# Performance work log

Hardware: AMD Instinct MI355X
Metric: run time of the kernel (lower is better)

Reference implementation:

```python
import jax, jax.numpy as jnp
import numpy as np

GROUP = 32  # quantization group size along K, fixed by the call site


def setup_inputs() -> dict:
    key = jax.random.key(0)
    k1, k2, k3 = jax.random.split(key, 3)
    M, K, N = 1, 8192, 16384
    A = jax.random.normal(k1, (M, K), dtype=jnp.float16)
    # packed int4 weights: each byte holds two nibbles -> [N, K//2]
    B = jax.random.randint(k2, (N, K // 2), 0, 256, dtype=jnp.int32)
    scalesAndZeros = (jax.random.normal(k3, (N, K // GROUP, 2), dtype=jnp.float16))
    return {"A": A, "B": B, "scalesAndZeros": scalesAndZeros}


def _dequant(B, scalesAndZeros):
    # B: [N, K//2] bytes, two int4 values per byte (low nibble = even k)
    N, Kh = B.shape
    K = Kh * 2
    low = B & 0xF
    high = (B >> 4) & 0xF
    q = jnp.stack([low, high], axis=-1).reshape(N, K).astype(jnp.float32) - 8.0
    scales = scalesAndZeros[..., 0].astype(jnp.float32)  # [N, K//GROUP]
    zeros = scalesAndZeros[..., 1].astype(jnp.float32)   # [N, K//GROUP]
    qg = q.reshape(N, K // GROUP, GROUP)
    W = qg * scales[:, :, None] + zeros[:, :, None]       # [N, K//GROUP, GROUP]
    return W.reshape(N, K)


def reference(A, B, scalesAndZeros):
    # int4 weight-only quantized GEMV: out[m, n] = sum_k A[m, k] * dequant(W)[n, k]
    W = _dequant(B, scalesAndZeros)                        # [N, K] fp32
    out = jnp.einsum("mk,nk->mn", A.astype(jnp.float32), W)
    return out.astype(A.dtype)                             # [1, N] fp16
```

## Files before the change

kernel.cpp:

```cpp
#include <hip/hip_runtime.h>


#define TPB   512
#define ROWS  2
#define TILES 16
#define CROWS (ROWS * TILES)

typedef int   ivec4 __attribute__((ext_vector_type(4)));
typedef float fvec2 __attribute__((ext_vector_type(2)));

__global__ __launch_bounds__(TPB, 4) void gemv_w4pipe(
    const float4* __restrict__ A4,
    const ivec4*  __restrict__ B,
    const fvec2*  __restrict__ SZ,
    float* __restrict__ out,
    int N)
{
    const int t    = threadIdx.x;
    const int row0 = blockIdx.x * CROWS;
    const int g0   = t >> 2;

    __shared__ fvec2 sz_s[2][ROWS * 256];
    __shared__ float red[2][ROWS][TPB / 64];

    float a[2][8];
    float sA[2];
#pragma unroll
    for (int j = 0; j < 2; ++j) {
        const int i = t + 512 * j;
        const float4 x = A4[2 * i];
        const float4 y = A4[2 * i + 1];
        a[j][0] = x.x; a[j][1] = x.y; a[j][2] = x.z; a[j][3] = x.w;
        a[j][4] = y.x; a[j][5] = y.y; a[j][6] = y.z; a[j][7] = y.w;
        sA[j] = ((x.x + x.y) + (x.z + x.w)) + ((y.x + y.y) + (y.z + y.w));
    }

    ivec4 bufA[ROWS][2], bufB[ROWS][2];
    fvec2 szrA, szrB;

    auto issue = [&](int T, ivec4 (&buf)[ROWS][2], fvec2& szr) {
        const int rt = row0 + T * ROWS;
        szr = __builtin_nontemporal_load(&SZ[(size_t)rt * 256 + t]);
        const ivec4* Bp = B + (size_t)rt * 1024 + t;
#pragma unroll
        for (int r = 0; r < ROWS; ++r)
#pragma unroll
            for (int j = 0; j < 2; ++j)
                buf[r][j] = __builtin_nontemporal_load(&Bp[r * 1024 + 512 * j]);
    };

    auto consume = [&](const ivec4 (&buf)[ROWS][2], const fvec2* szl,
                       float (&redb)[ROWS][TPB / 64]) {
        float acc[ROWS];
#pragma unroll
        for (int r = 0; r < ROWS; ++r) acc[r] = 0.0f;
#pragma unroll
        for (int r = 0; r < ROWS; ++r) {
#pragma unroll
            for (int j = 0; j < 2; ++j) {
                const fvec2 sz = szl[r * 256 + g0 + 128 * j];
                const int b0 = buf[r][j][0], b1 = buf[r][j][1];
                const int b2 = buf[r][j][2], b3 = buf[r][j][3];
                float dot = 0.0f;
                dot = fmaf(a[j][0], (float)(b0 & 0xF),        dot);
                dot = fmaf(a[j][1], (float)((b0 >> 4) & 0xF), dot);
                dot = fmaf(a[j][2], (float)(b1 & 0xF),        dot);
                dot = fmaf(a[j][3], (float)((b1 >> 4) & 0xF), dot);
                dot = fmaf(a[j][4], (float)(b2 & 0xF),        dot);
                dot = fmaf(a[j][5], (float)((b2 >> 4) & 0xF), dot);
                dot = fmaf(a[j][6], (float)(b3 & 0xF),        dot);
                dot = fmaf(a[j][7], (float)((b3 >> 4) & 0xF), dot);
                acc[r] = fmaf(sz[0], dot, acc[r]);
                acc[r] = fmaf(fmaf(-8.0f, sz[0], sz[1]), sA[j], acc[r]);
            }
        }
        const int lane = t & 63;
        const int w    = t >> 6;
#pragma unroll
        for (int r = 0; r < ROWS; ++r) {
            float v = acc[r];
#pragma unroll
            for (int off = 32; off > 0; off >>= 1)
                v += __shfl_down(v, off, 64);
            if (lane == 0) redb[r][w] = v;
        }
    };

    auto store2 = [&](int T, const float (&redb)[ROWS][TPB / 64]) {
        if (t < ROWS) {
            const int n = row0 + T * ROWS + t;
            if (n < N) {
                float v = 0.0f;
#pragma unroll
                for (int w2 = 0; w2 < TPB / 64; ++w2) v += redb[t][w2];
                out[n] = v;
            }
        }
    };

    issue(0, bufA, szrA);
    sz_s[0][t] = szrA;
    __syncthreads();

    for (int TT = 0; TT < TILES; TT += 2) {
        if (TT + 1 < TILES) issue(TT + 1, bufB, szrB);
        consume(bufA, &sz_s[0][0], red[0]);
        if (TT + 1 < TILES) sz_s[1][t] = szrB;
        __syncthreads();
        store2(TT, red[0]);

        if (TT + 2 < TILES) issue(TT + 2, bufA, szrA);
        consume(bufB, &sz_s[1][0], red[1]);
        if (TT + 2 < TILES) sz_s[0][t] = szrA;
        __syncthreads();
        store2(TT + 1, red[1]);
    }
}

extern "C" void kernel_launch(void* const* d_in, const int* in_sizes, int n_in,
                              void* d_out, int out_size, void* d_ws, size_t ws_size,
                              hipStream_t stream) {
    const float4* A4 = (const float4*)d_in[0];
    const ivec4*  B  = (const ivec4*)d_in[1];
    const fvec2*  SZ = (const fvec2*)d_in[2];
    float* out = (float*)d_out;

    const int N = out_size;
    gemv_w4pipe<<<N / CROWS, TPB, 0, stream>>>(A4, B, SZ, out, N);
}
```

Baseline: 351.5 us.

## Replace LDS-staged scales and per-tile barriers with register double-buffered asm loads

Scales and zeros are now loaded straight into registers by each thread instead of being staged through shared memory. The per-tile __syncthreads barriers are removed, leaving a single barrier before a final 32-row reduction. Weight and scale loads go through inline asm (nontemporal dwordx4 and dwordx2) with explicit vmcnt waits, so two tiles stay in flight per thread. This aims to cut barrier stalls and LDS traffic, at the cost of redundant scale loads across threads and a fragile hand-counted vmcnt scheme.

```diff
diff --git a/kernel.cpp b/kernel.cpp
--- a/kernel.cpp
+++ b/kernel.cpp
@@ -9,7 +9,14 @@
 typedef int   ivec4 __attribute__((ext_vector_type(4)));
 typedef float fvec2 __attribute__((ext_vector_type(2)));
 
-__global__ __launch_bounds__(TPB, 4) void gemv_w4pipe(
+#define NT16(dst, p) asm volatile("global_load_dwordx4 %0, %1, off sc0 sc1 nt" \
+                                  : "=v"(dst) : "v"(p) : "memory")
+#define LD8(dst, p)  asm volatile("global_load_dwordx2 %0, %1, off"            \
+                                  : "=v"(dst) : "v"(p) : "memory")
+#define WAITV(n)     do { asm volatile("s_waitcnt vmcnt(" n ")" ::: "memory"); \
+                          __builtin_amdgcn_sched_barrier(0); } while (0)
+
+__global__ __launch_bounds__(TPB, 4) void gemv_w4str(
     const float4* __restrict__ A4,
     const ivec4*  __restrict__ B,
     const fvec2*  __restrict__ SZ,
@@ -17,14 +24,15 @@
     int N)
 {
     const int t    = threadIdx.x;
+    const int lane = t & 63;
+    const int w    = t >> 6;
     const int row0 = blockIdx.x * CROWS;
     const int g0   = t >> 2;
 
-    __shared__ fvec2 sz_s[2][ROWS * 256];
-    __shared__ float red[2][ROWS][TPB / 64];
+    __shared__ float red2[CROWS][8];
 
     float a[2][8];
-    float sA[2];
+    float sAv[2];
 #pragma unroll
     for (int j = 0; j < 2; ++j) {
         const int i = t + 512 * j;
@@ -32,25 +40,27 @@
         const float4 y = A4[2 * i + 1];
         a[j][0] = x.x; a[j][1] = x.y; a[j][2] = x.z; a[j][3] = x.w;
         a[j][4] = y.x; a[j][5] = y.y; a[j][6] = y.z; a[j][7] = y.w;
-        sA[j] = ((x.x + x.y) + (x.z + x.w)) + ((y.x + y.y) + (y.z + y.w));
+        sAv[j] = ((x.x + x.y) + (x.z + x.w)) + ((y.x + y.y) + (y.z + y.w));
     }
 
-    ivec4 bufA[ROWS][2], bufB[ROWS][2];
-    fvec2 szrA, szrB;
+    ivec4 bA[4], bB[4];
+    fvec2 szA[4], szB[4];
 
-    auto issue = [&](int T, ivec4 (&buf)[ROWS][2], fvec2& szr) {
+    auto issue = [&](int T, ivec4 (&b)[4], fvec2 (&sz)[4]) {
         const int rt = row0 + T * ROWS;
-        szr = __builtin_nontemporal_load(&SZ[(size_t)rt * 256 + t]);
         const ivec4* Bp = B + (size_t)rt * 1024 + t;
-#pragma unroll
-        for (int r = 0; r < ROWS; ++r)
-#pragma unroll
-            for (int j = 0; j < 2; ++j)
-                buf[r][j] = __builtin_nontemporal_load(&Bp[r * 1024 + 512 * j]);
+        NT16(b[0], Bp);
+        NT16(b[1], Bp + 512);
+        NT16(b[2], Bp + 1024);
+        NT16(b[3], Bp + 1536);
+        const fvec2* Sp = SZ + (size_t)rt * 256 + g0;
+        LD8(sz[0], Sp);
+        LD8(sz[1], Sp + 128);
+        LD8(sz[2], Sp + 256);
+        LD8(sz[3], Sp + 384);
     };
 
-    auto consume = [&](const ivec4 (&buf)[ROWS][2], const fvec2* szl,
-                       float (&redb)[ROWS][TPB / 64]) {
+    auto consume = [&](const ivec4 (&b)[4], const fvec2 (&sz)[4], int rr) {
         float acc[ROWS];
 #pragma unroll
         for (int r = 0; r < ROWS; ++r) acc[r] = 0.0f;
@@ -58,62 +68,54 @@
         for (int r = 0; r < ROWS; ++r) {
 #pragma unroll
             for (int j = 0; j < 2; ++j) {
-                const fvec2 sz = szl[r * 256 + g0 + 128 * j];
-                const int b0 = buf[r][j][0], b1 = buf[r][j][1];
-                const int b2 = buf[r][j][2], b3 = buf[r][j][3];
+                const ivec4 bb = b[r * 2 + j];
+                const fvec2 ss = sz[r * 2 + j];
+                const int c0 = bb[0], c1 = bb[1], c2 = bb[2], c3 = bb[3];
                 float dot = 0.0f;
-                dot = fmaf(a[j][0], (float)(b0 & 0xF),        dot);
-                dot = fmaf(a[j][1], (float)((b0 >> 4) & 0xF), dot);
-                dot = fmaf(a[j][2], (float)(b1 & 0xF),        dot);
-                dot = fmaf(a[j][3], (float)((b1 >> 4) & 0xF), dot);
-                dot = fmaf(a[j][4], (float)(b2 & 0xF),        dot);
-                dot = fmaf(a[j][5], (float)((b2 >> 4) & 0xF), dot);
-                dot = fmaf(a[j][6], (float)(b3 & 0xF),        dot);
-                dot = fmaf(a[j][7], (float)((b3 >> 4) & 0xF), dot);
-                acc[r] = fmaf(sz[0], dot, acc[r]);
-                acc[r] = fmaf(fmaf(-8.0f, sz[0], sz[1]), sA[j], acc[r]);
+                dot = fmaf(a[j][0], (float)(c0 & 0xF),        dot);
+                dot = fmaf(a[j][1], (float)((c0 >> 4) & 0xF), dot);
+                dot = fmaf(a[j][2], (float)(c1 & 0xF),        dot);
+                dot = fmaf(a[j][3], (float)((c1 >> 4) & 0xF), dot);
+                dot = fmaf(a[j][4], (float)(c2 & 0xF),        dot);
+                dot = fmaf(a[j][5], (float)((c2 >> 4) & 0xF), dot);
+                dot = fmaf(a[j][6], (float)(c3 & 0xF),        dot);
+                dot = fmaf(a[j][7], (float)((c3 >> 4) & 0xF), dot);
+                acc[r] = fmaf(ss[0], dot, acc[r]);
+                acc[r] = fmaf(fmaf(-8.0f, ss[0], ss[1]), sAv[j], acc[r]);
             }
         }
-        const int lane = t & 63;
-        const int w    = t >> 6;
 #pragma unroll
         for (int r = 0; r < ROWS; ++r) {
             float v = acc[r];
 #pragma unroll
             for (int off = 32; off > 0; off >>= 1)
                 v += __shfl_down(v, off, 64);
-            if (lane == 0) redb[r][w] = v;
+            if (lane == 0) red2[rr + r][w] = v;
         }
     };
 
-    auto store2 = [&](int T, const float (&redb)[ROWS][TPB / 64]) {
-        if (t < ROWS) {
-            const int n = row0 + T * ROWS + t;
-            if (n < N) {
-                float v = 0.0f;
-#pragma unroll
-                for (int w2 = 0; w2 < TPB / 64; ++w2) v += redb[t][w2];
-                out[n] = v;
-            }
-        }
-    };
-
-    issue(0, bufA, szrA);
-    sz_s[0][t] = szrA;
-    __syncthreads();
+    issue(0, bA, szA);
+    issue(1, bB, szB);
 
     for (int TT = 0; TT < TILES; TT += 2) {
-        if (TT + 1 < TILES) issue(TT + 1, bufB, szrB);
-        consume(bufA, &sz_s[0][0], red[0]);
-        if (TT + 1 < TILES) sz_s[1][t] = szrB;
-        __syncthreads();
-        store2(TT, red[0]);
+        WAITV("8");
+        consume(bA, szA, TT * ROWS);
+        if (TT + 2 < TILES) issue(TT + 2, bA, szA);
 
-        if (TT + 2 < TILES) issue(TT + 2, bufA, szrA);
-        consume(bufB, &sz_s[1][0], red[1]);
-        if (TT + 2 < TILES) sz_s[0][t] = szrA;
-        __syncthreads();
-        store2(TT + 1, red[1]);
+        if (TT + 2 < TILES) WAITV("8"); else WAITV("0");
+        consume(bB, szB, (TT + 1) * ROWS);
+        if (TT + 3 < TILES) issue(TT + 3, bB, szB);
+    }
+
+    __syncthreads();
+    if (t < CROWS) {
+        const int n = row0 + t;
+        if (n < N) {
+            float v = 0.0f;
+#pragma unroll
+            for (int w2 = 0; w2 < 8; ++w2) v += red2[t][w2];
+            out[n] = v;
+        }
     }
 }
 
@@ -126,5 +128,5 @@
     float* out = (float*)d_out;
 
     const int N = out_size;
-    gemv_w4pipe<<<N / CROWS, TPB, 0, stream>>>(A4, B, SZ, out, N);
+    gemv_w4str<<<N / CROWS, TPB, 0, stream>>>(A4, B, SZ, out, N);
 }
```

Result: slower. 367.4 us (+4.5%).
